# Optimization experiments

Measured on AMD Instinct MI355X. Metric: run time of the kernel, lower is better.

Reference implementation:

```python
import jax, jax.numpy as jnp
import numpy as np
import math

B, T, D_MODEL, H = 2, 2048, 1024, 16
HD = D_MODEL // H  # head_dim = 64


def setup_inputs() -> dict:
    key = jax.random.key(0)
    ks = jax.random.split(key, 9)
    inp = {
        "x_q": jax.random.normal(ks[0], (B, T, D_MODEL), dtype=jnp.float32),
        "x_k": jax.random.normal(ks[1], (B, T, D_MODEL), dtype=jnp.float32),
        "x_v": jax.random.normal(ks[2], (B, T, D_MODEL), dtype=jnp.float32),
        "mask": jax.random.randint(ks[3], (B, T), 0, 2, dtype=jnp.int32),
        "causal": 1,
        "relative_position_bias": jax.random.normal(ks[4], (1, H, T, T), dtype=jnp.float32),
        "Wq": jax.random.normal(ks[5], (D_MODEL, D_MODEL), dtype=jnp.float32) * 0.02,
        "Wk": jax.random.normal(ks[6], (D_MODEL, D_MODEL), dtype=jnp.float32) * 0.02,
        "Wv": jax.random.normal(ks[7], (D_MODEL, D_MODEL), dtype=jnp.float32) * 0.02,
        "Wo": jax.random.normal(ks[8], (D_MODEL, D_MODEL), dtype=jnp.float32) * 0.02,
    }
    return inp


def _split_heads(x):
    b, t, _ = x.shape
    return x.reshape(b, t, H, HD).transpose(0, 2, 1, 3)  # (B, H, T, HD)


def reference(x_q, x_k, x_v, mask, causal, relative_position_bias, Wq, Wk, Wv, Wo):
    # torch.nn.Linear: y = x @ W.T
    q = _split_heads(x_q @ Wq.T)
    k = _split_heads(x_k @ Wk.T)
    v = _split_heads(x_v @ Wv.T)

    # padding mask (B, T_k) -> (B, 1, 1, T_k), combined with causal tril
    attn_mask = mask[:, None, None, :]
    if causal:
        tril = jnp.tril(jnp.ones((T, T), dtype=jnp.int32))[None, None]
        attn_mask = attn_mask & tril

    scores = jnp.einsum('bhqd,bhkd->bhqk', q, k) / math.sqrt(HD)
    scores = scores + relative_position_bias
    scores = jnp.where(attn_mask == 0, jnp.float32(-1e9), scores)
    attn = jax.nn.softmax(scores, axis=-1)  # (B, H, Tq, Tk)

    out_h = jnp.einsum('bhqk,bhkd->bhqd', attn, v)
    out = out_h.transpose(0, 2, 1, 3).reshape(B, T, D_MODEL)
    out = out @ Wo.T
    return out, attn
```

## Files before the change

### kernel.cpp

```cpp
#include <hip/hip_runtime.h>
#include <hip/hip_bf16.h>
#include <hip/hip_fp16.h>

#define B_ 2
#define T_ 2048
#define DM 1024
#define H_ 16
#define HD_ 64

typedef __attribute__((ext_vector_type(8))) short bf16x8v;
typedef __attribute__((ext_vector_type(4))) short short4v;
typedef __attribute__((ext_vector_type(4))) float f32x4;

__device__ __forceinline__ short f2bf(float f){
  unsigned u = __builtin_bit_cast(unsigned, f);
  u += 0x7fffu + ((u >> 16) & 1u);
  return (short)(u >> 16);
}
__device__ __forceinline__ float bf2f(short s){
  unsigned u = ((unsigned)(unsigned short)s) << 16;
  return __builtin_bit_cast(float, u);
}

#define GLOAD_LDS16(g, l) \
  __builtin_amdgcn_global_load_lds((const __attribute__((address_space(1))) unsigned int*)(g), \
                                   (__attribute__((address_space(3))) unsigned int*)(l), 16, 0, 0)

#define MFMA16(a, b, c) __builtin_amdgcn_mfma_f32_16x16x32_bf16((a), (b), (c), 0, 0, 0)

__global__ __launch_bounds__(256) void conv_kernel(
    const float* __restrict__ s0, const float* __restrict__ s1, const float* __restrict__ s2,
    const float* __restrict__ s3, const float* __restrict__ s4, const float* __restrict__ s5,
    const float* __restrict__ s6,
    short* __restrict__ d0, short* __restrict__ d1, short* __restrict__ d2,
    short* __restrict__ d3, short* __restrict__ d4, short* __restrict__ d5,
    short* __restrict__ d6)
{
  int y = blockIdx.y;
  const float* s; short* d; int n;
  switch (y) {
    case 0: s = s0; d = d0; n = B_*T_*DM; break;
    case 1: s = s1; d = d1; n = B_*T_*DM; break;
    case 2: s = s2; d = d2; n = B_*T_*DM; break;
    case 3: s = s3; d = d3; n = DM*DM;   break;
    case 4: s = s4; d = d4; n = DM*DM;   break;
    case 5: s = s5; d = d5; n = DM*DM;   break;
    default: s = s6; d = d6; n = DM*DM;  break;
  }
  int i = (blockIdx.x * 256 + threadIdx.x) * 4;
  if (i >= n) return;
  float4 f = *(const float4*)(s + i);
  short4v o;
  o.x = f2bf(f.x); o.y = f2bf(f.y); o.z = f2bf(f.z); o.w = f2bf(f.w);
  *(short4v*)(d + i) = o;
}

__global__ __launch_bounds__(256) void proj_gemm(
    const short* __restrict__ xq, const short* __restrict__ xk, const short* __restrict__ xv,
    const short* __restrict__ wq, const short* __restrict__ wk, const short* __restrict__ wv,
    short* __restrict__ qo, short* __restrict__ ko, short* __restrict__ vto)
{
  __shared__ short As[128 * 32];
  __shared__ short Bs[128 * 32];
  const int z = blockIdx.z;
  const short* A  = (z == 0) ? xq : (z == 1) ? xk : xv;
  const short* Bw = (z == 0) ? wq : (z == 1) ? wk : wv;
  const int m0 = blockIdx.x * 128;
  const int n0 = blockIdx.y * 128;
  const int tid = threadIdx.x;
  const int w = tid >> 6, l = tid & 63;
  const int wr = w >> 1, wc = w & 1;
  const int fr = l & 15, kq8 = (l >> 4) * 8;
  const int srow = tid >> 2, scol = (tid & 3) * 8;

  f32x4 acc[4][4] = {};

  for (int k0 = 0; k0 < DM; k0 += 32) {
    __syncthreads();
    GLOAD_LDS16(A  + (size_t)(m0 + srow) * DM + k0 + scol,      (char*)As + tid * 16);
    GLOAD_LDS16(A  + (size_t)(m0 + 64 + srow) * DM + k0 + scol, (char*)As + 4096 + tid * 16);
    GLOAD_LDS16(Bw + (size_t)(n0 + srow) * DM + k0 + scol,      (char*)Bs + tid * 16);
    GLOAD_LDS16(Bw + (size_t)(n0 + 64 + srow) * DM + k0 + scol, (char*)Bs + 4096 + tid * 16);
    __syncthreads();
    bf16x8v a[4], b[4];
#pragma unroll
    for (int i = 0; i < 4; i++) a[i] = *(const bf16x8v*)&As[(wr * 64 + i * 16 + fr) * 32 + kq8];
#pragma unroll
    for (int j = 0; j < 4; j++) b[j] = *(const bf16x8v*)&Bs[(wc * 64 + j * 16 + fr) * 32 + kq8];
#pragma unroll
    for (int i = 0; i < 4; i++)
#pragma unroll
      for (int j = 0; j < 4; j++)
        acc[i][j] = MFMA16(a[i], b[j], acc[i][j]);
  }

  const float scale = (z == 0) ? 0.125f : 1.0f;
  short* dst01 = (z == 0) ? qo : ko;
#pragma unroll
  for (int i = 0; i < 4; i++) {
#pragma unroll
    for (int j = 0; j < 4; j++) {
#pragma unroll
      for (int r = 0; r < 4; r++) {
        int row = m0 + wr * 64 + i * 16 + (l >> 4) * 4 + r;
        int col = n0 + wc * 64 + j * 16 + fr;
        int bb = row >> 11, tt = row & (T_ - 1);
        int hh = col >> 6,  hd = col & (HD_ - 1);
        short v = f2bf(acc[i][j][r] * scale);
        if (z == 2)
          vto[(((size_t)bb * H_ + hh) * HD_ + hd) * T_ + tt] = v;
        else
          dst01[(((size_t)bb * H_ + hh) * T_ + tt) * HD_ + hd] = v;
      }
    }
  }
}

__global__ __launch_bounds__(256) void vsum_kernel(const short* __restrict__ vt,
                                                   float* __restrict__ vs)
{
  __shared__ float red[256];
  int bh = blockIdx.x;
  int tid = threadIdx.x;
  int hd = tid & 63, part = tid >> 6;
  const short* src = vt + ((size_t)bh * HD_ + hd) * T_ + part * 512;
  float s = 0.f;
  for (int i = 0; i < 512; i += 4) {
    short4v v = *(const short4v*)(src + i);
    s += bf2f(v.x) + bf2f(v.y) + bf2f(v.z) + bf2f(v.w);
  }
  red[tid] = s;
  __syncthreads();
  if (part == 0)
    vs[(size_t)bh * HD_ + hd] = red[hd] + red[64 + hd] + red[128 + hd] + red[192 + hd];
}

__global__ __launch_bounds__(128, 4) void attn_kernel(
    const short* __restrict__ qw, const short* __restrict__ kw, const short* __restrict__ vt,
    const float* __restrict__ bias, const int* __restrict__ mask,
    const int* __restrict__ causal_p, const float* __restrict__ vsum,
    float* __restrict__ attn_out, short* __restrict__ outh)
{
  __shared__ float s_t[2][2][16][68];
  __shared__ float ml_l[2][2][16][2];
  __shared__ float mrow_l[2][16];
  float* pv = &s_t[0][0][0][0];

  const int tid = threadIdx.x;
  const int w = tid >> 6, l = tid & 63;
  const int fr = l & 15, q4 = l >> 4, kq8 = q4 * 8;
  const int wgid = blockIdx.x;
  const int h  = (wgid & 7) | (((wgid >> 3) & 1) << 3);
  const int jt = 127 - (wgid >> 4);
  const int q0w = jt * 16;
  const int causal = *causal_p;
  const int L = causal ? (q0w + 16) : T_;
  const int KEND = (L + 63) & ~63;
  const float invT = 1.0f / (float)T_;

  const short* Kb0 = kw + ((size_t)0 * H_ + h) * T_ * HD_;
  const short* Kb1 = kw + ((size_t)1 * H_ + h) * T_ * HD_;
  const short* Vb0 = vt + ((size_t)0 * H_ + h) * HD_ * T_;
  const short* Vb1 = vt + ((size_t)1 * H_ + h) * HD_ * T_;
  const float* biasb = bias + ((size_t)h * T_ + q0w) * T_;

  bf16x8v qa[2][2];
#pragma unroll
  for (int b = 0; b < 2; b++) {
    const short* qp = qw + (((size_t)b * H_ + h) * T_ + q0w + fr) * HD_;
    qa[b][0] = *(const bf16x8v*)(qp + kq8);
    qa[b][1] = *(const bf16x8v*)(qp + 32 + kq8);
  }

  float m4[2][4], l4[2][4];
#pragma unroll
  for (int b = 0; b < 2; b++)
#pragma unroll
    for (int r = 0; r < 4; r++) { m4[b][r] = -3e38f; l4[b][r] = 0.f; }

  for (int k0 = w * 64; k0 < KEND; k0 += 128) {
#pragma unroll
    for (int t = 0; t < 4; t++) {
      const int kcol = k0 + t * 16 + fr;
      bf16x8v kA0 = *(const bf16x8v*)(Kb0 + (size_t)kcol * HD_ + kq8);
      bf16x8v kA1 = *(const bf16x8v*)(Kb0 + (size_t)kcol * HD_ + 32 + kq8);
      bf16x8v kB0 = *(const bf16x8v*)(Kb1 + (size_t)kcol * HD_ + kq8);
      bf16x8v kB1 = *(const bf16x8v*)(Kb1 + (size_t)kcol * HD_ + 32 + kq8);
      float bi[4];
      const float* bp = biasb + (size_t)(q4 * 4) * T_ + kcol;
#pragma unroll
      for (int r = 0; r < 4; r++) bi[r] = bp[(size_t)r * T_];
      int mk0 = mask[kcol];
      int mk1 = mask[T_ + kcol];
      f32x4 s0 = {0.f, 0.f, 0.f, 0.f}, s1 = {0.f, 0.f, 0.f, 0.f};
      s0 = MFMA16(qa[0][0], kA0, s0); s0 = MFMA16(qa[0][1], kA1, s0);
      s1 = MFMA16(qa[1][0], kB0, s1); s1 = MFMA16(qa[1][1], kB1, s1);
#pragma unroll
      for (int r = 0; r < 4; r++) {
        bool cok = (!causal) || (kcol <= q0w + q4 * 4 + r);
        float sv0 = (mk0 && cok) ? (s0[r] + bi[r]) : -1e9f;
        float sv1 = (mk1 && cok) ? (s1[r] + bi[r]) : -1e9f;
        float d0 = sv0 - m4[0][r];
        float e0 = __expf(-fabsf(d0));
        l4[0][r] = (d0 > 0.f) ? (l4[0][r] * e0 + 1.f) : (l4[0][r] + e0);
        m4[0][r] = fmaxf(m4[0][r], sv0);
        float d1 = sv1 - m4[1][r];
        float e1 = __expf(-fabsf(d1));
        l4[1][r] = (d1 > 0.f) ? (l4[1][r] * e1 + 1.f) : (l4[1][r] + e1);
        m4[1][r] = fmaxf(m4[1][r], sv1);
      }
    }
  }
#pragma unroll
  for (int b = 0; b < 2; b++)
#pragma unroll
    for (int r = 0; r < 4; r++) {
#pragma unroll
      for (int off = 1; off < 16; off <<= 1) {
        float om = __shfl_xor(m4[b][r], off);
        float ol = __shfl_xor(l4[b][r], off);
        float nm = fmaxf(m4[b][r], om);
        l4[b][r] = l4[b][r] * __expf(m4[b][r] - nm) + ol * __expf(om - nm);
        m4[b][r] = nm;
      }
    }
  if (fr == 0) {
#pragma unroll
    for (int b = 0; b < 2; b++)
#pragma unroll
      for (int r = 0; r < 4; r++) {
        ml_l[w][b][q4 * 4 + r][0] = m4[b][r];
        ml_l[w][b][q4 * 4 + r][1] = l4[b][r];
      }
  }
  __syncthreads();

  float lse[2][4];
  bool fm[2][4];
#pragma unroll
  for (int b = 0; b < 2; b++)
#pragma unroll
    for (int r = 0; r < 4; r++) {
      int row = q4 * 4 + r;
      float ma = ml_l[0][b][row][0], la = ml_l[0][b][row][1];
      float mb = ml_l[1][b][row][0], lb = ml_l[1][b][row][1];
      float M = fmaxf(ma, mb);
      float lsum = la * __expf(ma - M) + lb * __expf(mb - M);
      fm[b][r] = (M <= -0.5e9f);
      lse[b][r] = M + __logf(lsum);
      if (fr == 0) mrow_l[b][row] = M;
    }

  f32x4 oacc[2][4] = {};
  for (int k0 = w * 64; k0 < KEND; k0 += 128) {
#pragma unroll
    for (int t = 0; t < 4; t++) {
      const int kcol = k0 + t * 16 + fr;
      bf16x8v kA0 = *(const bf16x8v*)(Kb0 + (size_t)kcol * HD_ + kq8);
      bf16x8v kA1 = *(const bf16x8v*)(Kb0 + (size_t)kcol * HD_ + 32 + kq8);
      bf16x8v kB0 = *(const bf16x8v*)(Kb1 + (size_t)kcol * HD_ + kq8);
      bf16x8v kB1 = *(const bf16x8v*)(Kb1 + (size_t)kcol * HD_ + 32 + kq8);
      float bi[4];
      const float* bp = biasb + (size_t)(q4 * 4) * T_ + kcol;
#pragma unroll
      for (int r = 0; r < 4; r++) bi[r] = bp[(size_t)r * T_];
      int mk0 = mask[kcol];
      int mk1 = mask[T_ + kcol];
      f32x4 s0 = {0.f, 0.f, 0.f, 0.f}, s1 = {0.f, 0.f, 0.f, 0.f};
      s0 = MFMA16(qa[0][0], kA0, s0); s0 = MFMA16(qa[0][1], kA1, s0);
      s1 = MFMA16(qa[1][0], kB0, s1); s1 = MFMA16(qa[1][1], kB1, s1);
#pragma unroll
      for (int r = 0; r < 4; r++) {
        bool cok = (!causal) || (kcol <= q0w + q4 * 4 + r);
        float sv0 = (mk0 && cok) ? (s0[r] + bi[r]) : -1e9f;
        float sv1 = (mk1 && cok) ? (s1[r] + bi[r]) : -1e9f;
        float p0 = fm[0][r] ? 0.f : __expf(sv0 - lse[0][r]);
        float p1 = fm[1][r] ? 0.f : __expf(sv1 - lse[1][r]);
        s_t[w][0][q4 * 4 + r][t * 16 + fr] = p0;
        s_t[w][1][q4 * 4 + r][t * 16 + fr] = p1;
      }
    }
#pragma unroll
    for (int b = 0; b < 2; b++) {
      float* arowb = attn_out + (((size_t)b * H_ + h) * T_ + q0w) * T_;
#pragma unroll
      for (int jj = 0; jj < 4; jj++) {
        int row = 4 * jj + q4;
        f32x4 pvv = *(const f32x4*)&s_t[w][b][row][fr * 4];
        bool fmj = mrow_l[b][row] <= -0.5e9f;
        f32x4 ov;
        ov[0] = fmj ? invT : pvv[0];
        ov[1] = fmj ? invT : pvv[1];
        ov[2] = fmj ? invT : pvv[2];
        ov[3] = fmj ? invT : pvv[3];
        __builtin_nontemporal_store(ov, (f32x4*)(arowb + (size_t)row * T_ + k0 + fr * 4));
      }
      const short* Vbb = b ? Vb1 : Vb0;
#pragma unroll
      for (int ks = 0; ks < 2; ks++) {
        f32x4 pa0 = *(const f32x4*)&s_t[w][b][fr][ks * 32 + kq8];
        f32x4 pa1 = *(const f32x4*)&s_t[w][b][fr][ks * 32 + kq8 + 4];
        bf16x8v pa;
#pragma unroll
        for (int i = 0; i < 4; i++) { pa[i] = f2bf(pa0[i]); pa[4 + i] = f2bf(pa1[i]); }
#pragma unroll
        for (int n0 = 0; n0 < 4; n0++) {
          bf16x8v vv = *(const bf16x8v*)&Vbb[(size_t)(n0 * 16 + fr) * T_ + k0 + ks * 32 + kq8];
          oacc[b][n0] = MFMA16(pa, vv, oacc[b][n0]);
        }
      }
    }
  }

  if (w == 0) {
#pragma unroll
    for (int b = 0; b < 2; b++)
#pragma unroll
      for (int n0 = 0; n0 < 4; n0++)
#pragma unroll
        for (int r = 0; r < 4; r++)
          pv[(b * 16 + q4 * 4 + r) * 64 + n0 * 16 + fr] = oacc[b][n0][r];
  }
  __syncthreads();
  if (w == 1) {
#pragma unroll
    for (int b = 0; b < 2; b++)
#pragma unroll
      for (int n0 = 0; n0 < 4; n0++)
#pragma unroll
        for (int r = 0; r < 4; r++) {
          int row = q4 * 4 + r, col = n0 * 16 + fr;
          float val = oacc[b][n0][r] + pv[(b * 16 + row) * 64 + col];
          if (fm[b][r]) val = vsum[((size_t)b * H_ + h) * HD_ + col] * invT;
          outh[(((size_t)b * H_ + h) * T_ + q0w + row) * HD_ + col] = f2bf(val);
        }
  } else if (KEND < T_) {
#pragma unroll
    for (int b = 0; b < 2; b++) {
      for (int row = 0; row < 16; row++) {
        float fill = (mrow_l[b][row] <= -0.5e9f) ? invT : 0.f;
        f32x4 fv = {fill, fill, fill, fill};
        float* rp = attn_out + (((size_t)b * H_ + h) * T_ + q0w + row) * T_;
        for (int c = KEND + l * 4; c < T_; c += 256)
          __builtin_nontemporal_store(fv, (f32x4*)(rp + c));
      }
    }
  }
}

__global__ __launch_bounds__(256) void out_gemm(
    const short* __restrict__ Ah, const short* __restrict__ Bw, float* __restrict__ Co)
{
  __shared__ short As[128 * 32];
  __shared__ short Bs[128 * 32];
  const int m0 = blockIdx.x * 128;
  const int n0 = blockIdx.y * 128;
  const int tid = threadIdx.x;
  const int w = tid >> 6, l = tid & 63;
  const int wr = w >> 1, wc = w & 1;
  const int fr = l & 15, kq8 = (l >> 4) * 8;
  const int srow = tid >> 2, scol = (tid & 3) * 8;

  f32x4 acc[4][4] = {};

  for (int k0 = 0; k0 < DM; k0 += 32) {
    __syncthreads();
    int kk = k0 + scol;
    int hh = kk >> 6, hd = kk & 63;
    {
      int m1 = m0 + srow;
      const short* src1 = Ah + (((size_t)(m1 >> 11) * H_ + hh) * T_ + (m1 & (T_ - 1))) * HD_ + hd;
      GLOAD_LDS16(src1, (char*)As + tid * 16);
      int m2 = m0 + 64 + srow;
      const short* src2 = Ah + (((size_t)(m2 >> 11) * H_ + hh) * T_ + (m2 & (T_ - 1))) * HD_ + hd;
      GLOAD_LDS16(src2, (char*)As + 4096 + tid * 16);
    }
    GLOAD_LDS16(Bw + (size_t)(n0 + srow) * DM + kk,      (char*)Bs + tid * 16);
    GLOAD_LDS16(Bw + (size_t)(n0 + 64 + srow) * DM + kk, (char*)Bs + 4096 + tid * 16);
    __syncthreads();
    bf16x8v a[4], b[4];
#pragma unroll
    for (int i = 0; i < 4; i++) a[i] = *(const bf16x8v*)&As[(wr * 64 + i * 16 + fr) * 32 + kq8];
#pragma unroll
    for (int j = 0; j < 4; j++) b[j] = *(const bf16x8v*)&Bs[(wc * 64 + j * 16 + fr) * 32 + kq8];
#pragma unroll
    for (int i = 0; i < 4; i++)
#pragma unroll
      for (int j = 0; j < 4; j++)
        acc[i][j] = MFMA16(a[i], b[j], acc[i][j]);
  }

#pragma unroll
  for (int i = 0; i < 4; i++)
#pragma unroll
    for (int j = 0; j < 4; j++)
#pragma unroll
      for (int r = 0; r < 4; r++) {
        int row = m0 + wr * 64 + i * 16 + (l >> 4) * 4 + r;
        int col = n0 + wc * 64 + j * 16 + fr;
        Co[(size_t)row * DM + col] = acc[i][j][r];
      }
}

extern "C" void kernel_launch(void* const* d_in, const int* in_sizes, int n_in,
                              void* d_out, int out_size, void* d_ws, size_t ws_size,
                              hipStream_t stream)
{
  const float* x_q  = (const float*)d_in[0];
  const float* x_k  = (const float*)d_in[1];
  const float* x_v  = (const float*)d_in[2];
  const int*   mask = (const int*)d_in[3];
  const int*   causal = (const int*)d_in[4];
  const float* bias = (const float*)d_in[5];
  const float* Wq   = (const float*)d_in[6];
  const float* Wk   = (const float*)d_in[7];
  const float* Wv   = (const float*)d_in[8];
  const float* Wo   = (const float*)d_in[9];

  char* ws = (char*)d_ws;
  const size_t XB = (size_t)B_ * T_ * DM * 2;
  const size_t WB = (size_t)DM * DM * 2;
  short* xq_b = (short*)(ws + 0 * XB);
  short* xk_b = (short*)(ws + 1 * XB);
  short* xv_b = (short*)(ws + 2 * XB);
  short* wq_b = (short*)(ws + 3 * XB + 0 * WB);
  short* wk_b = (short*)(ws + 3 * XB + 1 * WB);
  short* wv_b = (short*)(ws + 3 * XB + 2 * WB);
  short* wo_b = (short*)(ws + 3 * XB + 3 * WB);
  short* q_ws  = (short*)(ws + 3 * XB + 4 * WB);
  short* k_ws  = (short*)(ws + 4 * XB + 4 * WB);
  short* vt_ws = (short*)(ws + 5 * XB + 4 * WB);
  short* oh_ws = (short*)(ws + 6 * XB + 4 * WB);
  float* vs_ws = (float*)(ws + 7 * XB + 4 * WB);

  float* out0 = (float*)d_out;
  float* attn = out0 + (size_t)B_ * T_ * DM;

  conv_kernel<<<dim3(4096, 7, 1), 256, 0, stream>>>(
      x_q, x_k, x_v, Wq, Wk, Wv, Wo,
      xq_b, xk_b, xv_b, wq_b, wk_b, wv_b, wo_b);

  proj_gemm<<<dim3(32, 8, 3), 256, 0, stream>>>(
      xq_b, xk_b, xv_b, wq_b, wk_b, wv_b, q_ws, k_ws, vt_ws);

  vsum_kernel<<<dim3(32, 1, 1), 256, 0, stream>>>(vt_ws, vs_ws);

  attn_kernel<<<dim3(2048, 1, 1), 128, 0, stream>>>(
      q_ws, k_ws, vt_ws, bias, mask, causal, vs_ws, attn, oh_ws);

  out_gemm<<<dim3(32, 8, 1), 256, 0, stream>>>(oh_ws, wo_b, out0);
}
```

Baseline: 485.5 us.

## Transpose QK MFMA so each lane owns a query row with vectorized bias/mask loads

Swaps the QK^T MFMA operands so each lane holds scores for one query row across four consecutive keys. This lets bias and mask be read as 16-byte vectors and attention probabilities be stored straight from registers, without an fp32 LDS staging pass. The online softmax now works per 64-key block with a single max per block, fully unmasked tiles skip the causal check, P is staged in LDS as bf16, and both waves share the tail fill. The trade is an extra barrier and a different LDS access pattern that could cause bank conflicts.

```diff
diff --git a/kernel.cpp b/kernel.cpp
--- a/kernel.cpp
+++ b/kernel.cpp
@@ -141,10 +141,10 @@
     const int* __restrict__ causal_p, const float* __restrict__ vsum,
     float* __restrict__ attn_out, short* __restrict__ outh)
 {
-  __shared__ float s_t[2][2][16][68];
+  __shared__ short p_l[2][2][16][68];
   __shared__ float ml_l[2][2][16][2];
   __shared__ float mrow_l[2][16];
-  float* pv = &s_t[0][0][0][0];
+  float* pv = (float*)&p_l[0][0][0][0];
 
   const int tid = threadIdx.x;
   const int w = tid >> 6, l = tid & 63;
@@ -157,161 +157,169 @@
   const int L = causal ? (q0w + 16) : T_;
   const int KEND = (L + 63) & ~63;
   const float invT = 1.0f / (float)T_;
+  const int qrow = q0w + fr;
 
   const short* Kb0 = kw + ((size_t)0 * H_ + h) * T_ * HD_;
   const short* Kb1 = kw + ((size_t)1 * H_ + h) * T_ * HD_;
   const short* Vb0 = vt + ((size_t)0 * H_ + h) * HD_ * T_;
   const short* Vb1 = vt + ((size_t)1 * H_ + h) * HD_ * T_;
-  const float* biasb = bias + ((size_t)h * T_ + q0w) * T_;
+  const float* brow = bias + ((size_t)h * T_ + qrow) * T_;
 
   bf16x8v qa[2][2];
 #pragma unroll
   for (int b = 0; b < 2; b++) {
-    const short* qp = qw + (((size_t)b * H_ + h) * T_ + q0w + fr) * HD_;
+    const short* qp = qw + (((size_t)b * H_ + h) * T_ + qrow) * HD_;
     qa[b][0] = *(const bf16x8v*)(qp + kq8);
     qa[b][1] = *(const bf16x8v*)(qp + 32 + kq8);
   }
 
-  float m4[2][4], l4[2][4];
-#pragma unroll
-  for (int b = 0; b < 2; b++)
-#pragma unroll
-    for (int r = 0; r < 4; r++) { m4[b][r] = -3e38f; l4[b][r] = 0.f; }
+  float m_[2] = {-3e38f, -3e38f}, l_[2] = {0.f, 0.f};
 
   for (int k0 = w * 64; k0 < KEND; k0 += 128) {
+    f32x4 sv[2][4];
 #pragma unroll
     for (int t = 0; t < 4; t++) {
-      const int kcol = k0 + t * 16 + fr;
-      bf16x8v kA0 = *(const bf16x8v*)(Kb0 + (size_t)kcol * HD_ + kq8);
-      bf16x8v kA1 = *(const bf16x8v*)(Kb0 + (size_t)kcol * HD_ + 32 + kq8);
-      bf16x8v kB0 = *(const bf16x8v*)(Kb1 + (size_t)kcol * HD_ + kq8);
-      bf16x8v kB1 = *(const bf16x8v*)(Kb1 + (size_t)kcol * HD_ + 32 + kq8);
-      float bi[4];
-      const float* bp = biasb + (size_t)(q4 * 4) * T_ + kcol;
-#pragma unroll
-      for (int r = 0; r < 4; r++) bi[r] = bp[(size_t)r * T_];
-      int mk0 = mask[kcol];
-      int mk1 = mask[T_ + kcol];
-      f32x4 s0 = {0.f, 0.f, 0.f, 0.f}, s1 = {0.f, 0.f, 0.f, 0.f};
-      s0 = MFMA16(qa[0][0], kA0, s0); s0 = MFMA16(qa[0][1], kA1, s0);
-      s1 = MFMA16(qa[1][0], kB0, s1); s1 = MFMA16(qa[1][1], kB1, s1);
-#pragma unroll
-      for (int r = 0; r < 4; r++) {
-        bool cok = (!causal) || (kcol <= q0w + q4 * 4 + r);
-        float sv0 = (mk0 && cok) ? (s0[r] + bi[r]) : -1e9f;
-        float sv1 = (mk1 && cok) ? (s1[r] + bi[r]) : -1e9f;
-        float d0 = sv0 - m4[0][r];
-        float e0 = __expf(-fabsf(d0));
-        l4[0][r] = (d0 > 0.f) ? (l4[0][r] * e0 + 1.f) : (l4[0][r] + e0);
-        m4[0][r] = fmaxf(m4[0][r], sv0);
-        float d1 = sv1 - m4[1][r];
-        float e1 = __expf(-fabsf(d1));
-        l4[1][r] = (d1 > 0.f) ? (l4[1][r] * e1 + 1.f) : (l4[1][r] + e1);
-        m4[1][r] = fmaxf(m4[1][r], sv1);
-      }
-    }
-  }
-#pragma unroll
-  for (int b = 0; b < 2; b++)
-#pragma unroll
-    for (int r = 0; r < 4; r++) {
-#pragma unroll
-      for (int off = 1; off < 16; off <<= 1) {
-        float om = __shfl_xor(m4[b][r], off);
-        float ol = __shfl_xor(l4[b][r], off);
-        float nm = fmaxf(m4[b][r], om);
-        l4[b][r] = l4[b][r] * __expf(m4[b][r] - nm) + ol * __expf(om - nm);
-        m4[b][r] = nm;
-      }
-    }
-  if (fr == 0) {
-#pragma unroll
-    for (int b = 0; b < 2; b++)
-#pragma unroll
-      for (int r = 0; r < 4; r++) {
-        ml_l[w][b][q4 * 4 + r][0] = m4[b][r];
-        ml_l[w][b][q4 * 4 + r][1] = l4[b][r];
-      }
+      const int kb = k0 + t * 16;
+      const short* kp0 = Kb0 + (size_t)(kb + fr) * HD_ + kq8;
+      const short* kp1 = Kb1 + (size_t)(kb + fr) * HD_ + kq8;
+      f32x4 a0 = {0.f, 0.f, 0.f, 0.f}, a1 = {0.f, 0.f, 0.f, 0.f};
+      a0 = MFMA16(*(const bf16x8v*)kp0,        qa[0][0], a0);
+      a0 = MFMA16(*(const bf16x8v*)(kp0 + 32), qa[0][1], a0);
+      a1 = MFMA16(*(const bf16x8v*)kp1,        qa[1][0], a1);
+      a1 = MFMA16(*(const bf16x8v*)(kp1 + 32), qa[1][1], a1);
+      f32x4 bi = *(const f32x4*)(brow + kb + q4 * 4);
+      int4 mk0 = *(const int4*)(mask + kb + q4 * 4);
+      int4 mk1 = *(const int4*)(mask + T_ + kb + q4 * 4);
+      int mka[4] = {mk0.x, mk0.y, mk0.z, mk0.w};
+      int mkb[4] = {mk1.x, mk1.y, mk1.z, mk1.w};
+      if (!causal || (kb + 15 <= q0w)) {
+#pragma unroll
+        for (int r = 0; r < 4; r++) {
+          sv[0][t][r] = mka[r] ? (a0[r] + bi[r]) : -1e9f;
+          sv[1][t][r] = mkb[r] ? (a1[r] + bi[r]) : -1e9f;
+        }
+      } else {
+#pragma unroll
+        for (int r = 0; r < 4; r++) {
+          bool cok = (kb + q4 * 4 + r) <= qrow;
+          sv[0][t][r] = (mka[r] && cok) ? (a0[r] + bi[r]) : -1e9f;
+          sv[1][t][r] = (mkb[r] && cok) ? (a1[r] + bi[r]) : -1e9f;
+        }
+      }
+    }
+#pragma unroll
+    for (int b = 0; b < 2; b++) {
+      float tm = -3e38f;
+#pragma unroll
+      for (int t = 0; t < 4; t++)
+#pragma unroll
+        for (int r = 0; r < 4; r++) tm = fmaxf(tm, sv[b][t][r]);
+      float nm = fmaxf(m_[b], tm);
+      float ss = 0.f;
+#pragma unroll
+      for (int t = 0; t < 4; t++)
+#pragma unroll
+        for (int r = 0; r < 4; r++) ss += __expf(sv[b][t][r] - nm);
+      l_[b] = l_[b] * __expf(m_[b] - nm) + ss;
+      m_[b] = nm;
+    }
+  }
+#pragma unroll
+  for (int b = 0; b < 2; b++) {
+#pragma unroll
+    for (int off = 16; off < 64; off <<= 1) {
+      float om = __shfl_xor(m_[b], off);
+      float ol = __shfl_xor(l_[b], off);
+      float nm = fmaxf(m_[b], om);
+      l_[b] = l_[b] * __expf(m_[b] - nm) + ol * __expf(om - nm);
+      m_[b] = nm;
+    }
+  }
+  if (q4 == 0) {
+#pragma unroll
+    for (int b = 0; b < 2; b++) {
+      ml_l[w][b][fr][0] = m_[b];
+      ml_l[w][b][fr][1] = l_[b];
+    }
   }
   __syncthreads();
 
-  float lse[2][4];
-  bool fm[2][4];
-#pragma unroll
-  for (int b = 0; b < 2; b++)
-#pragma unroll
-    for (int r = 0; r < 4; r++) {
-      int row = q4 * 4 + r;
-      float ma = ml_l[0][b][row][0], la = ml_l[0][b][row][1];
-      float mb = ml_l[1][b][row][0], lb = ml_l[1][b][row][1];
-      float M = fmaxf(ma, mb);
-      float lsum = la * __expf(ma - M) + lb * __expf(mb - M);
-      fm[b][r] = (M <= -0.5e9f);
-      lse[b][r] = M + __logf(lsum);
-      if (fr == 0) mrow_l[b][row] = M;
-    }
+  float lse[2];
+  bool fm[2];
+#pragma unroll
+  for (int b = 0; b < 2; b++) {
+    float ma = ml_l[0][b][fr][0], la = ml_l[0][b][fr][1];
+    float mb = ml_l[1][b][fr][0], lb = ml_l[1][b][fr][1];
+    float M = fmaxf(ma, mb);
+    float lsum = la * __expf(ma - M) + lb * __expf(mb - M);
+    fm[b] = (M <= -0.5e9f);
+    lse[b] = M + __logf(lsum);
+    if (q4 == 0 && w == 0) mrow_l[b][fr] = M;
+  }
 
   f32x4 oacc[2][4] = {};
   for (int k0 = w * 64; k0 < KEND; k0 += 128) {
 #pragma unroll
     for (int t = 0; t < 4; t++) {
-      const int kcol = k0 + t * 16 + fr;
-      bf16x8v kA0 = *(const bf16x8v*)(Kb0 + (size_t)kcol * HD_ + kq8);
-      bf16x8v kA1 = *(const bf16x8v*)(Kb0 + (size_t)kcol * HD_ + 32 + kq8);
-      bf16x8v kB0 = *(const bf16x8v*)(Kb1 + (size_t)kcol * HD_ + kq8);
-      bf16x8v kB1 = *(const bf16x8v*)(Kb1 + (size_t)kcol * HD_ + 32 + kq8);
-      float bi[4];
-      const float* bp = biasb + (size_t)(q4 * 4) * T_ + kcol;
-#pragma unroll
-      for (int r = 0; r < 4; r++) bi[r] = bp[(size_t)r * T_];
-      int mk0 = mask[kcol];
-      int mk1 = mask[T_ + kcol];
-      f32x4 s0 = {0.f, 0.f, 0.f, 0.f}, s1 = {0.f, 0.f, 0.f, 0.f};
-      s0 = MFMA16(qa[0][0], kA0, s0); s0 = MFMA16(qa[0][1], kA1, s0);
-      s1 = MFMA16(qa[1][0], kB0, s1); s1 = MFMA16(qa[1][1], kB1, s1);
+      const int kb = k0 + t * 16;
+      const short* kp0 = Kb0 + (size_t)(kb + fr) * HD_ + kq8;
+      const short* kp1 = Kb1 + (size_t)(kb + fr) * HD_ + kq8;
+      f32x4 a0 = {0.f, 0.f, 0.f, 0.f}, a1 = {0.f, 0.f, 0.f, 0.f};
+      a0 = MFMA16(*(const bf16x8v*)kp0,        qa[0][0], a0);
+      a0 = MFMA16(*(const bf16x8v*)(kp0 + 32), qa[0][1], a0);
+      a1 = MFMA16(*(const bf16x8v*)kp1,        qa[1][0], a1);
+      a1 = MFMA16(*(const bf16x8v*)(kp1 + 32), qa[1][1], a1);
+      f32x4 bi = *(const f32x4*)(brow + kb + q4 * 4);
+      int4 mk0 = *(const int4*)(mask + kb + q4 * 4);
+      int4 mk1 = *(const int4*)(mask + T_ + kb + q4 * 4);
+      int mka[4] = {mk0.x, mk0.y, mk0.z, mk0.w};
+      int mkb[4] = {mk1.x, mk1.y, mk1.z, mk1.w};
+      f32x4 p0, p1;
+      if (!causal || (kb + 15 <= q0w)) {
+#pragma unroll
+        for (int r = 0; r < 4; r++) {
+          p0[r] = mka[r] ? __expf(a0[r] + bi[r] - lse[0]) : 0.f;
+          p1[r] = mkb[r] ? __expf(a1[r] + bi[r] - lse[1]) : 0.f;
+        }
+      } else {
+#pragma unroll
+        for (int r = 0; r < 4; r++) {
+          bool cok = (kb + q4 * 4 + r) <= qrow;
+          p0[r] = (mka[r] && cok) ? __expf(a0[r] + bi[r] - lse[0]) : 0.f;
+          p1[r] = (mkb[r] && cok) ? __expf(a1[r] + bi[r] - lse[1]) : 0.f;
+        }
+      }
+      f32x4 st0, st1;
 #pragma unroll
       for (int r = 0; r < 4; r++) {
-        bool cok = (!causal) || (kcol <= q0w + q4 * 4 + r);
-        float sv0 = (mk0 && cok) ? (s0[r] + bi[r]) : -1e9f;
-        float sv1 = (mk1 && cok) ? (s1[r] + bi[r]) : -1e9f;
-        float p0 = fm[0][r] ? 0.f : __expf(sv0 - lse[0][r]);
-        float p1 = fm[1][r] ? 0.f : __expf(sv1 - lse[1][r]);
-        s_t[w][0][q4 * 4 + r][t * 16 + fr] = p0;
-        s_t[w][1][q4 * 4 + r][t * 16 + fr] = p1;
-      }
-    }
-#pragma unroll
-    for (int b = 0; b < 2; b++) {
-      float* arowb = attn_out + (((size_t)b * H_ + h) * T_ + q0w) * T_;
-#pragma unroll
-      for (int jj = 0; jj < 4; jj++) {
-        int row = 4 * jj + q4;
-        f32x4 pvv = *(const f32x4*)&s_t[w][b][row][fr * 4];
-        bool fmj = mrow_l[b][row] <= -0.5e9f;
-        f32x4 ov;
-        ov[0] = fmj ? invT : pvv[0];
-        ov[1] = fmj ? invT : pvv[1];
-        ov[2] = fmj ? invT : pvv[2];
-        ov[3] = fmj ? invT : pvv[3];
-        __builtin_nontemporal_store(ov, (f32x4*)(arowb + (size_t)row * T_ + k0 + fr * 4));
-      }
-      const short* Vbb = b ? Vb1 : Vb0;
-#pragma unroll
-      for (int ks = 0; ks < 2; ks++) {
-        f32x4 pa0 = *(const f32x4*)&s_t[w][b][fr][ks * 32 + kq8];
-        f32x4 pa1 = *(const f32x4*)&s_t[w][b][fr][ks * 32 + kq8 + 4];
-        bf16x8v pa;
-#pragma unroll
-        for (int i = 0; i < 4; i++) { pa[i] = f2bf(pa0[i]); pa[4 + i] = f2bf(pa1[i]); }
-#pragma unroll
-        for (int n0 = 0; n0 < 4; n0++) {
-          bf16x8v vv = *(const bf16x8v*)&Vbb[(size_t)(n0 * 16 + fr) * T_ + k0 + ks * 32 + kq8];
-          oacc[b][n0] = MFMA16(pa, vv, oacc[b][n0]);
-        }
-      }
-    }
-  }
-
+        st0[r] = fm[0] ? invT : p0[r];
+        st1[r] = fm[1] ? invT : p1[r];
+      }
+      __builtin_nontemporal_store(st0,
+          (f32x4*)(attn_out + (((size_t)0 * H_ + h) * T_ + qrow) * T_ + kb + q4 * 4));
+      __builtin_nontemporal_store(st1,
+          (f32x4*)(attn_out + (((size_t)1 * H_ + h) * T_ + qrow) * T_ + kb + q4 * 4));
+      short4v pb0, pb1;
+#pragma unroll
+      for (int r = 0; r < 4; r++) { pb0[r] = f2bf(p0[r]); pb1[r] = f2bf(p1[r]); }
+      *(short4v*)&p_l[w][0][fr][t * 16 + q4 * 4] = pb0;
+      *(short4v*)&p_l[w][1][fr][t * 16 + q4 * 4] = pb1;
+    }
+#pragma unroll
+    for (int ks = 0; ks < 2; ks++) {
+      bf16x8v pa0 = *(const bf16x8v*)&p_l[w][0][fr][ks * 32 + kq8];
+      bf16x8v pa1 = *(const bf16x8v*)&p_l[w][1][fr][ks * 32 + kq8];
+#pragma unroll
+      for (int n0 = 0; n0 < 4; n0++) {
+        bf16x8v vv0 = *(const bf16x8v*)&Vb0[(size_t)(n0 * 16 + fr) * T_ + k0 + ks * 32 + kq8];
+        bf16x8v vv1 = *(const bf16x8v*)&Vb1[(size_t)(n0 * 16 + fr) * T_ + k0 + ks * 32 + kq8];
+        oacc[0][n0] = MFMA16(pa0, vv0, oacc[0][n0]);
+        oacc[1][n0] = MFMA16(pa1, vv1, oacc[1][n0]);
+      }
+    }
+  }
+
+  __syncthreads();
   if (w == 0) {
 #pragma unroll
     for (int b = 0; b < 2; b++)
@@ -331,18 +339,24 @@
         for (int r = 0; r < 4; r++) {
           int row = q4 * 4 + r, col = n0 * 16 + fr;
           float val = oacc[b][n0][r] + pv[(b * 16 + row) * 64 + col];
-          if (fm[b][r]) val = vsum[((size_t)b * H_ + h) * HD_ + col] * invT;
+          if (mrow_l[b][row] <= -0.5e9f)
+            val = vsum[((size_t)b * H_ + h) * HD_ + col] * invT;
           outh[(((size_t)b * H_ + h) * T_ + q0w + row) * HD_ + col] = f2bf(val);
         }
-  } else if (KEND < T_) {
-#pragma unroll
-    for (int b = 0; b < 2; b++) {
-      for (int row = 0; row < 16; row++) {
-        float fill = (mrow_l[b][row] <= -0.5e9f) ? invT : 0.f;
-        f32x4 fv = {fill, fill, fill, fill};
-        float* rp = attn_out + (((size_t)b * H_ + h) * T_ + q0w + row) * T_;
-        for (int c = KEND + l * 4; c < T_; c += 256)
-          __builtin_nontemporal_store(fv, (f32x4*)(rp + c));
+  }
+
+  if (KEND < T_) {
+    float fill0 = fm[0] ? invT : 0.f;
+    float fill1 = fm[1] ? invT : 0.f;
+    f32x4 fv0 = {fill0, fill0, fill0, fill0};
+    f32x4 fv1 = {fill1, fill1, fill1, fill1};
+    float* r0 = attn_out + (((size_t)0 * H_ + h) * T_ + qrow) * T_;
+    float* r1 = attn_out + (((size_t)1 * H_ + h) * T_ + qrow) * T_;
+    for (int cb = KEND + w * 64; cb < T_; cb += 128) {
+#pragma unroll
+      for (int t = 0; t < 4; t++) {
+        __builtin_nontemporal_store(fv0, (f32x4*)(r0 + cb + t * 16 + q4 * 4));
+        __builtin_nontemporal_store(fv1, (f32x4*)(r1 + cb + t * 16 + q4 * 4));
       }
     }
   }
```

Result: faster. 455.8 us (-6.1%).
